# Performance work log

Measured on AMD Instinct MI355X. Metric: run time of the kernel, lower is better.

The kernel has to match this reference:

```python
import jax, jax.numpy as jnp
import numpy as np

EPS = 1e-5  # torch.nn.LayerNorm default


def _layer_norm(h, g, b):
    mu = jnp.mean(h, axis=-1, keepdims=True)
    var = jnp.mean(jnp.square(h - mu), axis=-1, keepdims=True)
    return (h - mu) * jax.lax.rsqrt(var + EPS) * g + b


def setup_inputs() -> dict:
    key = jax.random.key(0)
    ks = jax.random.split(key, 16)
    N, E, D, G, H = 100000, 3200000, 16, 64, 8
    x = jax.random.normal(ks[0], (N, D), dtype=jnp.float32)
    edge_index = jax.random.randint(ks[1], (2, E), 0, N, dtype=jnp.int64)
    vp = jax.random.normal(ks[2], (G, D), dtype=jnp.float32)
    batch = jnp.sort(jax.random.randint(ks[3], (N,), 0, G, dtype=jnp.int64))
    def lin(k, fan_in, fan_out):
        bound = 1.0 / np.sqrt(fan_in)
        kw, kb = jax.random.split(k)
        W = jax.random.uniform(kw, (fan_in, fan_out), jnp.float32, -bound, bound)
        b = jax.random.uniform(kb, (fan_out,), jnp.float32, -bound, bound)
        return W, b
    W1, b1 = lin(ks[4], 3 * D, H)
    W2, b2 = lin(ks[5], H, H)
    W3, b3 = lin(ks[6], H, H)
    W4, b4 = lin(ks[7], H, 1)
    g1 = jnp.ones((H,), jnp.float32); be1 = jnp.zeros((H,), jnp.float32)
    g2 = jnp.ones((H,), jnp.float32); be2 = jnp.zeros((H,), jnp.float32)
    g3 = jnp.ones((H,), jnp.float32); be3 = jnp.zeros((H,), jnp.float32)
    return dict(x=x, edge_index=edge_index, vp=vp, batch=batch,
                W1=W1, b1=b1, g1=g1, be1=be1,
                W2=W2, b2=b2, g2=g2, be2=be2,
                W3=W3, b3=b3, g3=g3, be3=be3,
                W4=W4, b4=b4)


def reference(x, edge_index, vp, batch,
              W1, b1, g1, be1, W2, b2, g2, be2, W3, b3, g3, be3, W4, b4):
    start, end = edge_index[0], edge_index[1]
    # gather node features for both endpoints + per-graph features of the start node's event
    edge_inputs = jnp.concatenate([x[start], x[end], vp[batch[start]]], axis=1)  # [E, 3D]
    h = jnp.tanh(_layer_norm(edge_inputs @ W1 + b1, g1, be1))
    h = jnp.tanh(_layer_norm(h @ W2 + b2, g2, be2))
    h = jnp.tanh(_layer_norm(h @ W3 + b3, g3, be3))
    out = h @ W4 + b4  # [E, 1]
    return out.squeeze(-1)
```

## Files before the change

kernel.cpp:

```cpp
#include <hip/hip_runtime.h>


typedef __attribute__((ext_vector_type(8))) _Float16 h8;

__device__ __forceinline__ float fast_tanh(float v) {
    float e = __expf(2.0f * v);
    return fmaf(-2.0f, __builtin_amdgcn_rcpf(e + 1.0f), 1.0f);
}

__global__ __launch_bounds__(256) void node_pre_kernel(
    const float* __restrict__ x,
    const int* __restrict__ batch,
    const float* __restrict__ vp,
    const float* __restrict__ W1,
    const float* __restrict__ b1,
    h8* __restrict__ ya16,
    h8* __restrict__ yb16,
    int N)
{
    int n = blockIdx.x * blockDim.x + threadIdx.x;
    if (n >= N) return;

    const float4* px = reinterpret_cast<const float4*>(x) + (size_t)n * 4;
    float4 x0 = px[0], x1 = px[1], x2 = px[2], x3 = px[3];
    int g = batch[n];
    const float4* pv = reinterpret_cast<const float4*>(vp) + (size_t)g * 4;
    float4 v0 = pv[0], v1 = pv[1], v2 = pv[2], v3 = pv[3];

    float xs[16] = {x0.x, x0.y, x0.z, x0.w, x1.x, x1.y, x1.z, x1.w,
                    x2.x, x2.y, x2.z, x2.w, x3.x, x3.y, x3.z, x3.w};
    float vs[16] = {v0.x, v0.y, v0.z, v0.w, v1.x, v1.y, v1.z, v1.w,
                    v2.x, v2.y, v2.z, v2.w, v3.x, v3.y, v3.z, v3.w};

    float ya[8], yb[8];
#pragma unroll
    for (int j = 0; j < 8; ++j) { ya[j] = b1[j]; yb[j] = 0.0f; }

#pragma unroll
    for (int i = 0; i < 16; ++i) {
        float vx = xs[i];
        float vv = vs[i];
#pragma unroll
        for (int j = 0; j < 8; ++j) {
            ya[j] = fmaf(vx, W1[i * 8 + j], ya[j]);
            ya[j] = fmaf(vv, W1[(32 + i) * 8 + j], ya[j]);
            yb[j] = fmaf(vx, W1[(16 + i) * 8 + j], yb[j]);
        }
    }

    float mua = 0.0f, mub = 0.0f;
#pragma unroll
    for (int j = 0; j < 8; ++j) { mua += ya[j]; mub += yb[j]; }
    mua *= 0.125f; mub *= 0.125f;

    h8 va, vb;
#pragma unroll
    for (int j = 0; j < 8; ++j) {
        va[j] = (_Float16)(ya[j] - mua);
        vb[j] = (_Float16)(yb[j] - mub);
    }
    ya16[n] = va;
    yb16[n] = vb;
}

__global__ __launch_bounds__(256) void edge_main_kernel(
    const int* __restrict__ ei,
    const h8* __restrict__ ya16,
    const h8* __restrict__ yb16,
    const float* __restrict__ g1, const float* __restrict__ be1,
    const float* __restrict__ W2, const float* __restrict__ b2,
    const float* __restrict__ g2, const float* __restrict__ be2,
    const float* __restrict__ W3, const float* __restrict__ b3,
    const float* __restrict__ g3, const float* __restrict__ be3,
    const float* __restrict__ W4, const float* __restrict__ b4,
    float* __restrict__ out, int E)
{
    int e = blockIdx.x * blockDim.x + threadIdx.x;
    if (e >= E) return;

    int s = ei[e];
    int t = ei[E + e];

    h8 va = ya16[s];
    h8 vb = yb16[t];
    h8 vsum = va + vb;

    float h[8];
#pragma unroll
    for (int j = 0; j < 8; ++j) h[j] = (float)vsum[j];
    float ss = 0.0f;
#pragma unroll
    for (int j = 0; j < 8; ++j) ss = fmaf(h[j], h[j], ss);
    float r = __builtin_amdgcn_rsqf(fmaf(ss, 0.125f, 1e-5f));
#pragma unroll
    for (int j = 0; j < 8; ++j)
        h[j] = fast_tanh(fmaf(h[j], r * g1[j], be1[j]));

    float h2[8];
#pragma unroll
    for (int j = 0; j < 8; ++j) h2[j] = b2[j];
#pragma unroll
    for (int i = 0; i < 8; ++i) {
        float v = h[i];
#pragma unroll
        for (int j = 0; j < 8; ++j) h2[j] = fmaf(v, W2[i * 8 + j], h2[j]);
    }
    {
        float sm = 0.0f, sq = 0.0f;
#pragma unroll
        for (int j = 0; j < 8; ++j) { sm += h2[j]; sq = fmaf(h2[j], h2[j], sq); }
        float mu = sm * 0.125f;
        float var = fmaf(sq, 0.125f, -mu * mu);
        float rr = __builtin_amdgcn_rsqf(var + 1e-5f);
#pragma unroll
        for (int j = 0; j < 8; ++j)
            h2[j] = fast_tanh(fmaf(h2[j] - mu, rr * g2[j], be2[j]));
    }

    float h3[8];
#pragma unroll
    for (int j = 0; j < 8; ++j) h3[j] = b3[j];
#pragma unroll
    for (int i = 0; i < 8; ++i) {
        float v = h2[i];
#pragma unroll
        for (int j = 0; j < 8; ++j) h3[j] = fmaf(v, W3[i * 8 + j], h3[j]);
    }
    {
        float sm = 0.0f, sq = 0.0f;
#pragma unroll
        for (int j = 0; j < 8; ++j) { sm += h3[j]; sq = fmaf(h3[j], h3[j], sq); }
        float mu = sm * 0.125f;
        float var = fmaf(sq, 0.125f, -mu * mu);
        float rr = __builtin_amdgcn_rsqf(var + 1e-5f);
#pragma unroll
        for (int j = 0; j < 8; ++j)
            h3[j] = fast_tanh(fmaf(h3[j] - mu, rr * g3[j], be3[j]));
    }

    float o = b4[0];
#pragma unroll
    for (int i = 0; i < 8; ++i) o = fmaf(h3[i], W4[i], o);

    out[e] = o;
}

__device__ __forceinline__ void ln_tanh8_full(float* h, const float* __restrict__ g,
                                              const float* __restrict__ be) {
    float sm = 0.0f, sq = 0.0f;
#pragma unroll
    for (int j = 0; j < 8; ++j) { sm += h[j]; sq = fmaf(h[j], h[j], sq); }
    float mu = sm * 0.125f;
    float var = fmaf(sq, 0.125f, -mu * mu);
    float rr = __builtin_amdgcn_rsqf(var + 1e-5f);
#pragma unroll
    for (int j = 0; j < 8; ++j)
        h[j] = fast_tanh(fmaf(h[j] - mu, rr * g[j], be[j]));
}

__global__ __launch_bounds__(256) void edge_net_fallback(
    const float* __restrict__ x, const int* __restrict__ ei,
    const float* __restrict__ vp, const int* __restrict__ batch,
    const float* __restrict__ W1, const float* __restrict__ b1,
    const float* __restrict__ g1, const float* __restrict__ be1,
    const float* __restrict__ W2, const float* __restrict__ b2,
    const float* __restrict__ g2, const float* __restrict__ be2,
    const float* __restrict__ W3, const float* __restrict__ b3,
    const float* __restrict__ g3, const float* __restrict__ be3,
    const float* __restrict__ W4, const float* __restrict__ b4,
    float* __restrict__ out, int E)
{
    int e = blockIdx.x * blockDim.x + threadIdx.x;
    if (e >= E) return;
    int s = ei[e], t = ei[E + e];
    int gb = batch[s];
    float in[48];
    const float4* ps = reinterpret_cast<const float4*>(x) + (size_t)s * 4;
    const float4* pt = reinterpret_cast<const float4*>(x) + (size_t)t * 4;
    const float4* pv = reinterpret_cast<const float4*>(vp) + (size_t)gb * 4;
#pragma unroll
    for (int q = 0; q < 4; ++q) {
        float4 a = ps[q];
        in[q*4+0]=a.x; in[q*4+1]=a.y; in[q*4+2]=a.z; in[q*4+3]=a.w;
    }
#pragma unroll
    for (int q = 0; q < 4; ++q) {
        float4 a = pt[q];
        in[16+q*4+0]=a.x; in[16+q*4+1]=a.y; in[16+q*4+2]=a.z; in[16+q*4+3]=a.w;
    }
#pragma unroll
    for (int q = 0; q < 4; ++q) {
        float4 a = pv[q];
        in[32+q*4+0]=a.x; in[32+q*4+1]=a.y; in[32+q*4+2]=a.z; in[32+q*4+3]=a.w;
    }
    float h[8];
#pragma unroll
    for (int j = 0; j < 8; ++j) h[j] = b1[j];
#pragma unroll
    for (int i = 0; i < 48; ++i) {
        float v = in[i];
#pragma unroll
        for (int j = 0; j < 8; ++j) h[j] = fmaf(v, W1[i*8+j], h[j]);
    }
    ln_tanh8_full(h, g1, be1);
    float h2[8];
#pragma unroll
    for (int j = 0; j < 8; ++j) h2[j] = b2[j];
#pragma unroll
    for (int i = 0; i < 8; ++i) {
        float v = h[i];
#pragma unroll
        for (int j = 0; j < 8; ++j) h2[j] = fmaf(v, W2[i*8+j], h2[j]);
    }
    ln_tanh8_full(h2, g2, be2);
    float h3[8];
#pragma unroll
    for (int j = 0; j < 8; ++j) h3[j] = b3[j];
#pragma unroll
    for (int i = 0; i < 8; ++i) {
        float v = h2[i];
#pragma unroll
        for (int j = 0; j < 8; ++j) h3[j] = fmaf(v, W3[i*8+j], h3[j]);
    }
    ln_tanh8_full(h3, g3, be3);
    float o = b4[0];
#pragma unroll
    for (int i = 0; i < 8; ++i) o = fmaf(h3[i], W4[i], o);
    out[e] = o;
}

extern "C" void kernel_launch(void* const* d_in, const int* in_sizes, int n_in,
                              void* d_out, int out_size, void* d_ws, size_t ws_size,
                              hipStream_t stream) {
    const float* x     = (const float*)d_in[0];
    const int*   ei    = (const int*)d_in[1];
    const float* vp    = (const float*)d_in[2];
    const int*   batch = (const int*)d_in[3];
    const float* W1  = (const float*)d_in[4];
    const float* b1  = (const float*)d_in[5];
    const float* g1  = (const float*)d_in[6];
    const float* be1 = (const float*)d_in[7];
    const float* W2  = (const float*)d_in[8];
    const float* b2  = (const float*)d_in[9];
    const float* g2  = (const float*)d_in[10];
    const float* be2 = (const float*)d_in[11];
    const float* W3  = (const float*)d_in[12];
    const float* b3  = (const float*)d_in[13];
    const float* g3  = (const float*)d_in[14];
    const float* be3 = (const float*)d_in[15];
    const float* W4  = (const float*)d_in[16];
    const float* b4  = (const float*)d_in[17];

    int E = in_sizes[1] / 2;
    int N = in_sizes[3];
    float* out = (float*)d_out;

    size_t tab_bytes = (size_t)N * 8 * sizeof(_Float16);
    if (ws_size >= 2 * tab_bytes) {
        h8* ya16 = (h8*)d_ws;
        h8* yb16 = (h8*)((char*)d_ws + tab_bytes);
        int blockA = 256;
        int gridA = (N + blockA - 1) / blockA;
        hipLaunchKernelGGL(node_pre_kernel, dim3(gridA), dim3(blockA), 0, stream,
                           x, batch, vp, W1, b1, ya16, yb16, N);
        int blockB = 256;
        int gridB = (E + blockB - 1) / blockB;
        hipLaunchKernelGGL(edge_main_kernel, dim3(gridB), dim3(blockB), 0, stream,
                           ei, ya16, yb16, g1, be1, W2, b2, g2, be2,
                           W3, b3, g3, be3, W4, b4, out, E);
    } else {
        int block = 256;
        int grid = (E + block - 1) / block;
        hipLaunchKernelGGL(edge_net_fallback, dim3(grid), dim3(block), 0, stream,
                           x, ei, vp, batch,
                           W1, b1, g1, be1, W2, b2, g2, be2, W3, b3, g3, be3,
                           W4, b4, out, E);
    }
}
```

Before: 149.1 us.

## Compute edge MLP layers in packed half2 arithmetic with prepacked fp16 weights

Moves the per-edge LayerNorm statistics, affine steps and the two 8x8 matmuls from fp32 scalar FMAs to packed __half2 operations, which halves the ALU instruction count for those stages. A small pack kernel converts W2, W3, the biases and the LayerNorm gains and offsets to half2 once per call, storing them in workspace so the edge kernel reads one packed struct. Tanh stays in fp32. Accumulating sums of squares and matmul outputs in fp16 risks precision loss and overflow, and the extra launch adds a little overhead.

```diff
diff --git a/kernel.cpp b/kernel.cpp
--- a/kernel.cpp
+++ b/kernel.cpp
@@ -1,5 +1,15 @@
 #include <hip/hip_runtime.h>
-
+#include <hip/hip_fp16.h>
+
+
+struct WPack {
+    __half2 w2[32];
+    __half2 w3[32];
+    __half2 b2p[4], b3p[4];
+    __half2 g1p[4], be1p[4];
+    __half2 g2p[4], be2p[4];
+    __half2 g3p[4], be3p[4];
+};
 
 typedef __attribute__((ext_vector_type(8))) _Float16 h8;
 
@@ -63,15 +73,36 @@
     yb16[n] = vb;
 }
 
+__global__ void pack_kernel(
+    const float* __restrict__ W2, const float* __restrict__ b2,
+    const float* __restrict__ W3, const float* __restrict__ b3,
+    const float* __restrict__ g1, const float* __restrict__ be1,
+    const float* __restrict__ g2, const float* __restrict__ be2,
+    const float* __restrict__ g3, const float* __restrict__ be3,
+    WPack* __restrict__ wp)
+{
+    int t = threadIdx.x;
+    if (t < 32) {
+        wp->w2[t] = __floats2half2_rn(W2[2 * t], W2[2 * t + 1]);
+        wp->w3[t] = __floats2half2_rn(W3[2 * t], W3[2 * t + 1]);
+    }
+    if (t < 4) {
+        wp->b2p[t]  = __floats2half2_rn(b2[2 * t],  b2[2 * t + 1]);
+        wp->b3p[t]  = __floats2half2_rn(b3[2 * t],  b3[2 * t + 1]);
+        wp->g1p[t]  = __floats2half2_rn(g1[2 * t],  g1[2 * t + 1]);
+        wp->be1p[t] = __floats2half2_rn(be1[2 * t], be1[2 * t + 1]);
+        wp->g2p[t]  = __floats2half2_rn(g2[2 * t],  g2[2 * t + 1]);
+        wp->be2p[t] = __floats2half2_rn(be2[2 * t], be2[2 * t + 1]);
+        wp->g3p[t]  = __floats2half2_rn(g3[2 * t],  g3[2 * t + 1]);
+        wp->be3p[t] = __floats2half2_rn(be3[2 * t], be3[2 * t + 1]);
+    }
+}
+
 __global__ __launch_bounds__(256) void edge_main_kernel(
     const int* __restrict__ ei,
-    const h8* __restrict__ ya16,
-    const h8* __restrict__ yb16,
-    const float* __restrict__ g1, const float* __restrict__ be1,
-    const float* __restrict__ W2, const float* __restrict__ b2,
-    const float* __restrict__ g2, const float* __restrict__ be2,
-    const float* __restrict__ W3, const float* __restrict__ b3,
-    const float* __restrict__ g3, const float* __restrict__ be3,
+    const uint4* __restrict__ ya16,
+    const uint4* __restrict__ yb16,
+    const WPack* __restrict__ wp,
     const float* __restrict__ W4, const float* __restrict__ b4,
     float* __restrict__ out, int E)
 {
@@ -81,66 +112,108 @@
     int s = ei[e];
     int t = ei[E + e];
 
-    h8 va = ya16[s];
-    h8 vb = yb16[t];
-    h8 vsum = va + vb;
-
-    float h[8];
-#pragma unroll
-    for (int j = 0; j < 8; ++j) h[j] = (float)vsum[j];
-    float ss = 0.0f;
-#pragma unroll
-    for (int j = 0; j < 8; ++j) ss = fmaf(h[j], h[j], ss);
+    uint4 ua = ya16[s];
+    uint4 ub = yb16[t];
+    __half2 v[4];
+    {
+        const __half2* ha = reinterpret_cast<const __half2*>(&ua);
+        const __half2* hb2 = reinterpret_cast<const __half2*>(&ub);
+#pragma unroll
+        for (int k = 0; k < 4; ++k) v[k] = __hadd2(ha[k], hb2[k]);
+    }
+
+    __half2 s2 = __hmul2(v[0], v[0]);
+    s2 = __hfma2(v[1], v[1], s2);
+    s2 = __hfma2(v[2], v[2], s2);
+    s2 = __hfma2(v[3], v[3], s2);
+    float ss = __low2float(s2) + __high2float(s2);
     float r = __builtin_amdgcn_rsqf(fmaf(ss, 0.125f, 1e-5f));
-#pragma unroll
-    for (int j = 0; j < 8; ++j)
-        h[j] = fast_tanh(fmaf(h[j], r * g1[j], be1[j]));
-
-    float h2[8];
-#pragma unroll
-    for (int j = 0; j < 8; ++j) h2[j] = b2[j];
+    __half2 rr2 = __floats2half2_rn(r, r);
+
+    float th[8];
+    __half2 hb[8];
+#pragma unroll
+    for (int k = 0; k < 4; ++k) {
+        __half2 rg  = __hmul2(rr2, wp->g1p[k]);
+        __half2 arg = __hfma2(v[k], rg, wp->be1p[k]);
+        float a0 = fast_tanh(__low2float(arg));
+        float a1 = fast_tanh(__high2float(arg));
+        th[2 * k] = a0; th[2 * k + 1] = a1;
+        hb[2 * k]     = __floats2half2_rn(a0, a0);
+        hb[2 * k + 1] = __floats2half2_rn(a1, a1);
+    }
+
+    __half2 acc[4];
+#pragma unroll
+    for (int k = 0; k < 4; ++k) acc[k] = wp->b2p[k];
 #pragma unroll
     for (int i = 0; i < 8; ++i) {
-        float v = h[i];
-#pragma unroll
-        for (int j = 0; j < 8; ++j) h2[j] = fmaf(v, W2[i * 8 + j], h2[j]);
+#pragma unroll
+        for (int k = 0; k < 4; ++k)
+            acc[k] = __hfma2(hb[i], wp->w2[i * 4 + k], acc[k]);
     }
     {
-        float sm = 0.0f, sq = 0.0f;
-#pragma unroll
-        for (int j = 0; j < 8; ++j) { sm += h2[j]; sq = fmaf(h2[j], h2[j], sq); }
+        __half2 sm2 = __hadd2(__hadd2(acc[0], acc[1]), __hadd2(acc[2], acc[3]));
+        __half2 sq2 = __hmul2(acc[0], acc[0]);
+        sq2 = __hfma2(acc[1], acc[1], sq2);
+        sq2 = __hfma2(acc[2], acc[2], sq2);
+        sq2 = __hfma2(acc[3], acc[3], sq2);
+        float sm = __low2float(sm2) + __high2float(sm2);
+        float sq = __low2float(sq2) + __high2float(sq2);
         float mu = sm * 0.125f;
         float var = fmaf(sq, 0.125f, -mu * mu);
         float rr = __builtin_amdgcn_rsqf(var + 1e-5f);
-#pragma unroll
-        for (int j = 0; j < 8; ++j)
-            h2[j] = fast_tanh(fmaf(h2[j] - mu, rr * g2[j], be2[j]));
-    }
-
-    float h3[8];
-#pragma unroll
-    for (int j = 0; j < 8; ++j) h3[j] = b3[j];
+        __half2 rrp = __floats2half2_rn(rr, rr);
+        float m = -mu * rr;
+        __half2 mm2 = __floats2half2_rn(m, m);
+#pragma unroll
+        for (int k = 0; k < 4; ++k) {
+            __half2 rg  = __hmul2(rrp, wp->g2p[k]);
+            __half2 c   = __hfma2(mm2, wp->g2p[k], wp->be2p[k]);
+            __half2 arg = __hfma2(acc[k], rg, c);
+            float a0 = fast_tanh(__low2float(arg));
+            float a1 = fast_tanh(__high2float(arg));
+            th[2 * k] = a0; th[2 * k + 1] = a1;
+            hb[2 * k]     = __floats2half2_rn(a0, a0);
+            hb[2 * k + 1] = __floats2half2_rn(a1, a1);
+        }
+    }
+
+#pragma unroll
+    for (int k = 0; k < 4; ++k) acc[k] = wp->b3p[k];
 #pragma unroll
     for (int i = 0; i < 8; ++i) {
-        float v = h2[i];
-#pragma unroll
-        for (int j = 0; j < 8; ++j) h3[j] = fmaf(v, W3[i * 8 + j], h3[j]);
+#pragma unroll
+        for (int k = 0; k < 4; ++k)
+            acc[k] = __hfma2(hb[i], wp->w3[i * 4 + k], acc[k]);
     }
     {
-        float sm = 0.0f, sq = 0.0f;
-#pragma unroll
-        for (int j = 0; j < 8; ++j) { sm += h3[j]; sq = fmaf(h3[j], h3[j], sq); }
+        __half2 sm2 = __hadd2(__hadd2(acc[0], acc[1]), __hadd2(acc[2], acc[3]));
+        __half2 sq2 = __hmul2(acc[0], acc[0]);
+        sq2 = __hfma2(acc[1], acc[1], sq2);
+        sq2 = __hfma2(acc[2], acc[2], sq2);
+        sq2 = __hfma2(acc[3], acc[3], sq2);
+        float sm = __low2float(sm2) + __high2float(sm2);
+        float sq = __low2float(sq2) + __high2float(sq2);
         float mu = sm * 0.125f;
         float var = fmaf(sq, 0.125f, -mu * mu);
         float rr = __builtin_amdgcn_rsqf(var + 1e-5f);
-#pragma unroll
-        for (int j = 0; j < 8; ++j)
-            h3[j] = fast_tanh(fmaf(h3[j] - mu, rr * g3[j], be3[j]));
+        __half2 rrp = __floats2half2_rn(rr, rr);
+        float m = -mu * rr;
+        __half2 mm2 = __floats2half2_rn(m, m);
+#pragma unroll
+        for (int k = 0; k < 4; ++k) {
+            __half2 rg  = __hmul2(rrp, wp->g3p[k]);
+            __half2 c   = __hfma2(mm2, wp->g3p[k], wp->be3p[k]);
+            __half2 arg = __hfma2(acc[k], rg, c);
+            th[2 * k]     = fast_tanh(__low2float(arg));
+            th[2 * k + 1] = fast_tanh(__high2float(arg));
+        }
     }
 
     float o = b4[0];
 #pragma unroll
-    for (int i = 0; i < 8; ++i) o = fmaf(h3[i], W4[i], o);
+    for (int i = 0; i < 8; ++i) o = fmaf(th[i], W4[i], o);
 
     out[e] = o;
 }
@@ -256,18 +329,23 @@
     float* out = (float*)d_out;
 
     size_t tab_bytes = (size_t)N * 8 * sizeof(_Float16);
-    if (ws_size >= 2 * tab_bytes) {
+    size_t need = 2 * tab_bytes + sizeof(WPack) + 64;
+    if (ws_size >= need) {
         h8* ya16 = (h8*)d_ws;
         h8* yb16 = (h8*)((char*)d_ws + tab_bytes);
+        WPack* wp = (WPack*)((char*)d_ws + 2 * tab_bytes);
+
         int blockA = 256;
         int gridA = (N + blockA - 1) / blockA;
         hipLaunchKernelGGL(node_pre_kernel, dim3(gridA), dim3(blockA), 0, stream,
                            x, batch, vp, W1, b1, ya16, yb16, N);
+        hipLaunchKernelGGL(pack_kernel, dim3(1), dim3(64), 0, stream,
+                           W2, b2, W3, b3, g1, be1, g2, be2, g3, be3, wp);
         int blockB = 256;
         int gridB = (E + blockB - 1) / blockB;
         hipLaunchKernelGGL(edge_main_kernel, dim3(gridB), dim3(blockB), 0, stream,
-                           ei, ya16, yb16, g1, be1, W2, b2, g2, be2,
-                           W3, b3, g3, be3, W4, b4, out, E);
+                           ei, (const uint4*)ya16, (const uint4*)yb16, wp,
+                           W4, b4, out, E);
     } else {
         int block = 256;
         int grid = (E + block - 1) / block;
```

New measurement: 148.0 us. No clear change (-0.7%).
